# Performance work log

Measured on AMD Instinct MI355X. Metric: run time of the kernel, lower is better.

The kernel has to match this reference:

```python
import jax, jax.numpy as jnp
import numpy as np

B, S, D_IN, D_OUT, H = 16, 1024, 768, 768, 12
HD = D_OUT // H


def setup_inputs() -> dict:
    key = jax.random.key(0)
    ks = jax.random.split(key, 6)
    s_in = D_IN ** -0.5
    s_out = D_OUT ** -0.5
    return {
        "x": jax.random.normal(ks[0], (B, S, D_IN), dtype=jnp.float32),
        "w_q": jax.random.normal(ks[1], (D_IN, D_OUT), dtype=jnp.float32) * s_in,
        "w_k": jax.random.normal(ks[2], (D_IN, D_OUT), dtype=jnp.float32) * s_in,
        "w_v": jax.random.normal(ks[3], (D_IN, D_OUT), dtype=jnp.float32) * s_in,
        "w_o": jax.random.normal(ks[4], (D_OUT, D_OUT), dtype=jnp.float32) * s_out,
        "b_o": jax.random.normal(ks[5], (D_OUT,), dtype=jnp.float32) * 0.01,
    }


def reference(x, w_q, w_k, w_v, w_o, b_o):
    b, s, _ = x.shape
    # QKV projections (no bias), reshape to (b, h, s, hd)
    q = (x @ w_q).reshape(b, s, H, HD).transpose(0, 2, 1, 3)
    k = (x @ w_k).reshape(b, s, H, HD).transpose(0, 2, 1, 3)
    v = (x @ w_v).reshape(b, s, H, HD).transpose(0, 2, 1, 3)
    scale = HD ** -0.5
    scores = jnp.einsum("bhqd,bhkd->bhqk", q, k) * scale
    weights = jax.nn.softmax(scores, axis=-1)  # dropout p=0.0 -> identity
    ctx = jnp.einsum("bhqk,bhkd->bhqd", weights, v)
    ctx = ctx.transpose(0, 2, 1, 3).reshape(b, s, D_OUT)
    return ctx @ w_o + b_o
```

## Files before the change

### kernel.cpp

```cpp
#include <hip/hip_runtime.h>
#include <math.h>

#define BB 16
#define SS 1024
#define DIN 768
#define DOUT 768
#define NH 12
#define HDIM 64

typedef float  f32x4  __attribute__((ext_vector_type(4)));
typedef short  bf16x8 __attribute__((ext_vector_type(8)));
typedef unsigned short u16x4 __attribute__((ext_vector_type(4)));

__device__ __forceinline__ unsigned short f2b(float f) {
    union { float f; unsigned u; } v; v.f = f;
    unsigned r = v.u + 0x7FFFu + ((v.u >> 16) & 1u);
    return (unsigned short)(r >> 16);
}

__global__ __launch_bounds__(256) void k_convert_x(
    const float* __restrict__ x, unsigned short* __restrict__ xb, int n4)
{
    for (int i = blockIdx.x * 256 + threadIdx.x; i < n4; i += gridDim.x * 256) {
        float4 v = reinterpret_cast<const float4*>(x)[i];
        u16x4 o;
        o[0] = f2b(v.x); o[1] = f2b(v.y); o[2] = f2b(v.z); o[3] = f2b(v.w);
        reinterpret_cast<u16x4*>(xb)[i] = o;
    }
}

__global__ __launch_bounds__(256) void k_convert_w(
    const float* __restrict__ wq, const float* __restrict__ wk,
    const float* __restrict__ wv, const float* __restrict__ wo,
    unsigned short* __restrict__ wt, unsigned short* __restrict__ wot)
{
    __shared__ float T[64][65];
    const int z = blockIdx.z;
    const float* in = (z == 0) ? wq : (z == 1) ? wk : (z == 2) ? wv : wo;
    unsigned short* out = (z < 3) ? (wt + z * DIN * DOUT) : wot;

    const int k0 = blockIdx.x * 64;
    const int n0 = blockIdx.y * 64;
    const int tid = threadIdx.x;

    for (int i = tid; i < 4096; i += 256) {
        int r = i >> 6, c = i & 63;
        T[r][c] = in[(k0 + r) * DOUT + n0 + c];
    }
    __syncthreads();
    for (int i = tid; i < 4096; i += 256) {
        int r = i >> 6, c = i & 63;
        out[(n0 + r) * DIN + k0 + c] = f2b(T[c][r]);
    }
}

__global__ __launch_bounds__(256) void k_qkv_gemm(
    const unsigned short* __restrict__ A,
    const unsigned short* __restrict__ wt,
    unsigned short* __restrict__ qo, unsigned short* __restrict__ ko,
    unsigned short* __restrict__ vo)
{
    __shared__ unsigned short As[128 * 64];
    __shared__ unsigned short Bs[128 * 64];

    const int z = blockIdx.z;
    const unsigned short* Bt = wt + z * DIN * DOUT;
    unsigned short* outb = (z == 0) ? qo : (z == 1) ? ko : vo;

    const int tid  = threadIdx.x;
    const int lane = tid & 63;
    const int wid  = tid >> 6;
    const int wm   = wid >> 1, wn = wid & 1;
    const int lr   = lane & 15, lg = lane >> 4;

    const int m0 = blockIdx.x * 128;
    const int n0 = blockIdx.y * 128;

    f32x4 acc[4][4];
    #pragma unroll
    for (int i = 0; i < 4; ++i)
        #pragma unroll
        for (int j = 0; j < 4; ++j) acc[i][j] = (f32x4){0.f, 0.f, 0.f, 0.f};

    for (int kt = 0; kt < DIN / 64; ++kt) {
        const int k0 = kt * 64;
        #pragma unroll
        for (int t = 0; t < 4; ++t) {
            int c = tid + t * 256;
            int r = c >> 3, ch = c & 7;
            *reinterpret_cast<bf16x8*>(&As[(r << 6) + ((ch ^ (r & 7)) << 3)]) =
                *reinterpret_cast<const bf16x8*>(&A[(m0 + r) * DIN + k0 + (ch << 3)]);
            *reinterpret_cast<bf16x8*>(&Bs[(r << 6) + ((ch ^ (r & 7)) << 3)]) =
                *reinterpret_cast<const bf16x8*>(&Bt[(n0 + r) * DIN + k0 + (ch << 3)]);
        }
        __syncthreads();

        #pragma unroll
        for (int ks = 0; ks < 2; ++ks) {
            bf16x8 af[4], bfr[4];
            #pragma unroll
            for (int mi = 0; mi < 4; ++mi) {
                int r = wm * 64 + mi * 16 + lr;
                af[mi] = *reinterpret_cast<const bf16x8*>(
                    &As[(r << 6) + ((((ks << 2) + lg) ^ (r & 7)) << 3)]);
            }
            #pragma unroll
            for (int ni = 0; ni < 4; ++ni) {
                int r = wn * 64 + ni * 16 + lr;
                bfr[ni] = *reinterpret_cast<const bf16x8*>(
                    &Bs[(r << 6) + ((((ks << 2) + lg) ^ (r & 7)) << 3)]);
            }
            #pragma unroll
            for (int mi = 0; mi < 4; ++mi)
                #pragma unroll
                for (int ni = 0; ni < 4; ++ni)
                    acc[mi][ni] = __builtin_amdgcn_mfma_f32_16x16x32_bf16(
                        af[mi], bfr[ni], acc[mi][ni], 0, 0, 0);
        }
        __syncthreads();
    }

    #pragma unroll
    for (int mi = 0; mi < 4; ++mi) {
        #pragma unroll
        for (int rg = 0; rg < 4; ++rg) {
            int m = m0 + wm * 64 + mi * 16 + lg * 4 + rg;
            int b = m >> 10, s = m & 1023;
            #pragma unroll
            for (int ni = 0; ni < 4; ++ni) {
                int n = n0 + wn * 64 + ni * 16 + lr;
                int h = n >> 6, hd = n & 63;
                outb[((b * NH + h) * SS + s) * HDIM + hd] = f2b(acc[mi][ni][rg]);
            }
        }
    }
}

__global__ __launch_bounds__(256) void k_vtrans(
    const unsigned short* __restrict__ vb, unsigned short* __restrict__ vt)
{
    __shared__ unsigned short T[64 * 72];
    const int tid = threadIdx.x;
    const int st  = blockIdx.x;
    const int bh  = blockIdx.y;
    const int base = bh << 16;

    #pragma unroll
    for (int t = 0; t < 2; ++t) {
        int c = tid + t * 256;
        int s = c >> 3, d0 = (c & 7) << 3;
        *reinterpret_cast<bf16x8*>(&T[s * 72 + d0]) =
            *reinterpret_cast<const bf16x8*>(&vb[base + ((st * 64 + s) << 6) + d0]);
    }
    __syncthreads();
    #pragma unroll
    for (int t = 0; t < 2; ++t) {
        int c = tid + t * 256;
        int d = c >> 3, s0 = (c & 7) << 3;
        bf16x8 o;
        #pragma unroll
        for (int i = 0; i < 8; ++i) o[i] = (short)T[(s0 + i) * 72 + d];
        *reinterpret_cast<bf16x8*>(&vt[base + (d << 10) + st * 64 + s0]) = o;
    }
}

__global__ __launch_bounds__(256) void k_attn(
    const unsigned short* __restrict__ qb, const unsigned short* __restrict__ kb,
    const unsigned short* __restrict__ vt, unsigned short* __restrict__ ctxb)
{
    __shared__ unsigned short Qs[64 * 64];
    __shared__ unsigned short Ks[64 * 64];
    __shared__ unsigned short Vs[64 * 64];
    __shared__ unsigned short Ps[64 * 64];

    const int tid  = threadIdx.x;
    const int lane = tid & 63;
    const int w    = tid >> 6;
    const int lr   = lane & 15, lg = lane >> 4;
    const int qt   = blockIdx.x;
    const int bh   = blockIdx.y;
    const int b    = bh / NH, h = bh % NH;
    const int base = bh << 16;

    #pragma unroll
    for (int t = 0; t < 2; ++t) {
        int c = tid + t * 256;
        int r = c >> 3, ch = c & 7;
        *reinterpret_cast<bf16x8*>(&Qs[(r << 6) + ((ch ^ (r & 7)) << 3)]) =
            *reinterpret_cast<const bf16x8*>(&qb[base + ((qt * 64 + r) << 6) + (ch << 3)]);
    }

    float m_r[4], l_r[4];
    f32x4 ctx[4];
    #pragma unroll
    for (int i = 0; i < 4; ++i) {
        m_r[i] = -INFINITY; l_r[i] = 0.f;
        ctx[i] = (f32x4){0.f, 0.f, 0.f, 0.f};
    }

    for (int kt = 0; kt < 16; ++kt) {
        #pragma unroll
        for (int t = 0; t < 2; ++t) {
            int c = tid + t * 256;
            int r = c >> 3, ch = c & 7;
            *reinterpret_cast<bf16x8*>(&Ks[(r << 6) + ((ch ^ (r & 7)) << 3)]) =
                *reinterpret_cast<const bf16x8*>(&kb[base + ((kt * 64 + r) << 6) + (ch << 3)]);
            *reinterpret_cast<bf16x8*>(&Vs[(r << 6) + ((ch ^ (r & 7)) << 3)]) =
                *reinterpret_cast<const bf16x8*>(&vt[base + (r << 10) + (kt << 6) + (ch << 3)]);
        }
        __syncthreads();

        f32x4 sc[4];
        #pragma unroll
        for (int ni = 0; ni < 4; ++ni) sc[ni] = (f32x4){0.f, 0.f, 0.f, 0.f};
        #pragma unroll
        for (int ks = 0; ks < 2; ++ks) {
            int qrow = (w << 4) + lr;
            bf16x8 aq = *reinterpret_cast<const bf16x8*>(
                &Qs[(qrow << 6) + ((((ks << 2) + lg) ^ (qrow & 7)) << 3)]);
            #pragma unroll
            for (int ni = 0; ni < 4; ++ni) {
                int krow = (ni << 4) + lr;
                bf16x8 bk = *reinterpret_cast<const bf16x8*>(
                    &Ks[(krow << 6) + ((((ks << 2) + lg) ^ (krow & 7)) << 3)]);
                sc[ni] = __builtin_amdgcn_mfma_f32_16x16x32_bf16(aq, bk, sc[ni], 0, 0, 0);
            }
        }
        #pragma unroll
        for (int ni = 0; ni < 4; ++ni) sc[ni] *= 0.125f;

        #pragma unroll
        for (int rg = 0; rg < 4; ++rg) {
            float mx = fmaxf(fmaxf(sc[0][rg], sc[1][rg]),
                             fmaxf(sc[2][rg], sc[3][rg]));
            #pragma unroll
            for (int o = 1; o < 16; o <<= 1) mx = fmaxf(mx, __shfl_xor(mx, o));
            float mnew = fmaxf(m_r[rg], mx);
            float corr = __expf(m_r[rg] - mnew);
            float rs = 0.f;
            #pragma unroll
            for (int ni = 0; ni < 4; ++ni) {
                float p = __expf(sc[ni][rg] - mnew);
                sc[ni][rg] = p; rs += p;
            }
            #pragma unroll
            for (int o = 1; o < 16; o <<= 1) rs += __shfl_xor(rs, o);
            l_r[rg] = l_r[rg] * corr + rs;
            m_r[rg] = mnew;
            #pragma unroll
            for (int di = 0; di < 4; ++di) ctx[di][rg] *= corr;
        }

        #pragma unroll
        for (int rg = 0; rg < 4; ++rg) {
            int qr = (w << 4) + (lg << 2) + rg;
            #pragma unroll
            for (int ni = 0; ni < 4; ++ni) {
                int key = (ni << 4) + lr;
                Ps[(qr << 6) + ((((key >> 3) ^ (qr & 7)) << 3)) + (key & 7)]
                    = f2b(sc[ni][rg]);
            }
        }

        #pragma unroll
        for (int ks = 0; ks < 2; ++ks) {
            int prow = (w << 4) + lr;
            bf16x8 ap = *reinterpret_cast<const bf16x8*>(
                &Ps[(prow << 6) + ((((ks << 2) + lg) ^ (prow & 7)) << 3)]);
            #pragma unroll
            for (int di = 0; di < 4; ++di) {
                int vrow = (di << 4) + lr;
                bf16x8 bv = *reinterpret_cast<const bf16x8*>(
                    &Vs[(vrow << 6) + ((((ks << 2) + lg) ^ (vrow & 7)) << 3)]);
                ctx[di] = __builtin_amdgcn_mfma_f32_16x16x32_bf16(ap, bv, ctx[di], 0, 0, 0);
            }
        }
        __syncthreads();
    }

    #pragma unroll
    for (int rg = 0; rg < 4; ++rg) {
        float inv = 1.f / l_r[rg];
        int q = (qt << 6) + (w << 4) + (lg << 2) + rg;
        #pragma unroll
        for (int di = 0; di < 4; ++di) {
            int d = (di << 4) + lr;
            ctxb[(b * SS + q) * DOUT + h * HDIM + d] = f2b(ctx[di][rg] * inv);
        }
    }
}

__global__ __launch_bounds__(256) void k_out_gemm(
    const unsigned short* __restrict__ A,
    const unsigned short* __restrict__ Bt,
    const float* __restrict__ bo, float* __restrict__ out)
{
    __shared__ unsigned short As[128 * 64];
    __shared__ unsigned short Bs[128 * 64];

    const int tid  = threadIdx.x;
    const int lane = tid & 63;
    const int wid  = tid >> 6;
    const int wm   = wid >> 1, wn = wid & 1;
    const int lr   = lane & 15, lg = lane >> 4;

    const int m0 = blockIdx.x * 128;
    const int n0 = blockIdx.y * 128;

    f32x4 acc[4][4];
    #pragma unroll
    for (int i = 0; i < 4; ++i)
        #pragma unroll
        for (int j = 0; j < 4; ++j) acc[i][j] = (f32x4){0.f, 0.f, 0.f, 0.f};

    for (int kt = 0; kt < DOUT / 64; ++kt) {
        const int k0 = kt * 64;
        #pragma unroll
        for (int t = 0; t < 4; ++t) {
            int c = tid + t * 256;
            int r = c >> 3, ch = c & 7;
            *reinterpret_cast<bf16x8*>(&As[(r << 6) + ((ch ^ (r & 7)) << 3)]) =
                *reinterpret_cast<const bf16x8*>(&A[(m0 + r) * DOUT + k0 + (ch << 3)]);
            *reinterpret_cast<bf16x8*>(&Bs[(r << 6) + ((ch ^ (r & 7)) << 3)]) =
                *reinterpret_cast<const bf16x8*>(&Bt[(n0 + r) * DOUT + k0 + (ch << 3)]);
        }
        __syncthreads();

        #pragma unroll
        for (int ks = 0; ks < 2; ++ks) {
            bf16x8 af[4], bfr[4];
            #pragma unroll
            for (int mi = 0; mi < 4; ++mi) {
                int r = wm * 64 + mi * 16 + lr;
                af[mi] = *reinterpret_cast<const bf16x8*>(
                    &As[(r << 6) + ((((ks << 2) + lg) ^ (r & 7)) << 3)]);
            }
            #pragma unroll
            for (int ni = 0; ni < 4; ++ni) {
                int r = wn * 64 + ni * 16 + lr;
                bfr[ni] = *reinterpret_cast<const bf16x8*>(
                    &Bs[(r << 6) + ((((ks << 2) + lg) ^ (r & 7)) << 3)]);
            }
            #pragma unroll
            for (int mi = 0; mi < 4; ++mi)
                #pragma unroll
                for (int ni = 0; ni < 4; ++ni)
                    acc[mi][ni] = __builtin_amdgcn_mfma_f32_16x16x32_bf16(
                        af[mi], bfr[ni], acc[mi][ni], 0, 0, 0);
        }
        __syncthreads();
    }

    #pragma unroll
    for (int mi = 0; mi < 4; ++mi) {
        #pragma unroll
        for (int rg = 0; rg < 4; ++rg) {
            int m = m0 + wm * 64 + mi * 16 + lg * 4 + rg;
            #pragma unroll
            for (int ni = 0; ni < 4; ++ni) {
                int n = n0 + wn * 64 + ni * 16 + lr;
                out[m * DOUT + n] = acc[mi][ni][rg] + bo[n];
            }
        }
    }
}

extern "C" void kernel_launch(void* const* d_in, const int* in_sizes, int n_in,
                              void* d_out, int out_size, void* d_ws, size_t ws_size,
                              hipStream_t stream)
{
    const float* x  = (const float*)d_in[0];
    const float* wq = (const float*)d_in[1];
    const float* wk = (const float*)d_in[2];
    const float* wv = (const float*)d_in[3];
    const float* wo = (const float*)d_in[4];
    const float* bo = (const float*)d_in[5];
    float* out = (float*)d_out;

    const size_t N_X   = (size_t)BB * SS * DIN;
    const size_t N_W   = (size_t)DIN * DOUT;
    const size_t N_BHSD= (size_t)BB * NH * SS * HDIM;

    unsigned short* xb   = (unsigned short*)d_ws;
    unsigned short* wt   = xb   + N_X;
    unsigned short* wot  = wt   + 3 * N_W;
    unsigned short* qbuf = wot  + N_W;
    unsigned short* kbuf = qbuf + N_BHSD;
    unsigned short* vbuf = kbuf + N_BHSD;
    unsigned short* vtb  = vbuf + N_BHSD;
    unsigned short* ctxb = vtb  + N_BHSD;

    size_t need = (N_X + 4 * N_W + 5 * N_BHSD) * sizeof(unsigned short);
    if (ws_size < need) return;

    k_convert_x<<<4096, 256, 0, stream>>>(x, xb, (int)(N_X / 4));
    k_convert_w<<<dim3(12, 12, 4), 256, 0, stream>>>(wq, wk, wv, wo, wt, wot);
    k_qkv_gemm<<<dim3(128, 6, 3), 256, 0, stream>>>(xb, wt, qbuf, kbuf, vbuf);
    k_vtrans<<<dim3(16, 192), 256, 0, stream>>>(vbuf, vtb);
    k_attn<<<dim3(16, 192), 256, 0, stream>>>(qbuf, kbuf, vtb, ctxb);
    k_out_gemm<<<dim3(128, 6), 256, 0, stream>>>(ctxb, wot, bo, out);
}
```

Baseline: 401.0 us.

## Rework attention with 32x32 MFMA, direct-to-LDS loads, and fused V transpose

```diff
diff --git a/kernel.cpp b/kernel.cpp
--- a/kernel.cpp
+++ b/kernel.cpp
@@ -8,8 +8,9 @@
 #define NH 12
 #define HDIM 64
 
-typedef float  f32x4  __attribute__((ext_vector_type(4)));
-typedef short  bf16x8 __attribute__((ext_vector_type(8)));
+typedef float  f32x4   __attribute__((ext_vector_type(4)));
+typedef float  f32x16  __attribute__((ext_vector_type(16)));
+typedef short  bf16x8  __attribute__((ext_vector_type(8)));
 typedef unsigned short u16x4 __attribute__((ext_vector_type(4)));
 
 __device__ __forceinline__ unsigned short f2b(float f) {
@@ -17,6 +18,10 @@
     unsigned r = v.u + 0x7FFFu + ((v.u >> 16) & 1u);
     return (unsigned short)(r >> 16);
 }
+
+#define GLOAD16(gp, lp) __builtin_amdgcn_global_load_lds( \
+    (const __attribute__((address_space(1))) void*)(gp),  \
+    (__attribute__((address_space(3))) void*)(lp), 16, 0, 0)
 
 __global__ __launch_bounds__(256) void k_convert_x(
     const float* __restrict__ x, unsigned short* __restrict__ xb, int n4)
@@ -37,7 +42,7 @@
     __shared__ float T[64][65];
     const int z = blockIdx.z;
     const float* in = (z == 0) ? wq : (z == 1) ? wk : (z == 2) ? wv : wo;
-    unsigned short* out = (z < 3) ? (wt + z * DIN * DOUT) : wot;
+    unsigned short* out = (z < 3) ? (wt + (size_t)z * DIN * DOUT) : wot;
 
     const int k0 = blockIdx.x * 64;
     const int n0 = blockIdx.y * 64;
@@ -50,7 +55,7 @@
     __syncthreads();
     for (int i = tid; i < 4096; i += 256) {
         int r = i >> 6, c = i & 63;
-        out[(n0 + r) * DIN + k0 + c] = f2b(T[c][r]);
+        out[(size_t)(n0 + r) * DIN + k0 + c] = f2b(T[c][r]);
     }
 }
 
@@ -58,14 +63,13 @@
     const unsigned short* __restrict__ A,
     const unsigned short* __restrict__ wt,
     unsigned short* __restrict__ qo, unsigned short* __restrict__ ko,
-    unsigned short* __restrict__ vo)
+    unsigned short* __restrict__ vtb)
 {
     __shared__ unsigned short As[128 * 64];
     __shared__ unsigned short Bs[128 * 64];
 
     const int z = blockIdx.z;
-    const unsigned short* Bt = wt + z * DIN * DOUT;
-    unsigned short* outb = (z == 0) ? qo : (z == 1) ? ko : vo;
+    const unsigned short* Bt = wt + (size_t)z * DIN * DOUT;
 
     const int tid  = threadIdx.x;
     const int lane = tid & 63;
@@ -86,12 +90,13 @@
         const int k0 = kt * 64;
         #pragma unroll
         for (int t = 0; t < 4; ++t) {
-            int c = tid + t * 256;
-            int r = c >> 3, ch = c & 7;
-            *reinterpret_cast<bf16x8*>(&As[(r << 6) + ((ch ^ (r & 7)) << 3)]) =
-                *reinterpret_cast<const bf16x8*>(&A[(m0 + r) * DIN + k0 + (ch << 3)]);
-            *reinterpret_cast<bf16x8*>(&Bs[(r << 6) + ((ch ^ (r & 7)) << 3)]) =
-                *reinterpret_cast<const bf16x8*>(&Bt[(n0 + r) * DIN + k0 + (ch << 3)]);
+            int c  = t * 256 + wid * 64 + lane;
+            int r  = c >> 3;
+            int ch = (c & 7) ^ (r & 7);
+            GLOAD16(&A[(size_t)(m0 + r) * DIN + k0 + (ch << 3)],
+                    &As[(t * 256 + wid * 64) * 8]);
+            GLOAD16(&Bt[(size_t)(n0 + r) * DIN + k0 + (ch << 3)],
+                    &Bs[(t * 256 + wid * 64) * 8]);
         }
         __syncthreads();
 
@@ -120,6 +125,7 @@
         __syncthreads();
     }
 
+    const float oscale = (z == 0) ? 0.125f : 1.0f;
     #pragma unroll
     for (int mi = 0; mi < 4; ++mi) {
         #pragma unroll
@@ -130,37 +136,15 @@
             for (int ni = 0; ni < 4; ++ni) {
                 int n = n0 + wn * 64 + ni * 16 + lr;
                 int h = n >> 6, hd = n & 63;
-                outb[((b * NH + h) * SS + s) * HDIM + hd] = f2b(acc[mi][ni][rg]);
-            }
-        }
-    }
-}
-
-__global__ __launch_bounds__(256) void k_vtrans(
-    const unsigned short* __restrict__ vb, unsigned short* __restrict__ vt)
-{
-    __shared__ unsigned short T[64 * 72];
-    const int tid = threadIdx.x;
-    const int st  = blockIdx.x;
-    const int bh  = blockIdx.y;
-    const int base = bh << 16;
-
-    #pragma unroll
-    for (int t = 0; t < 2; ++t) {
-        int c = tid + t * 256;
-        int s = c >> 3, d0 = (c & 7) << 3;
-        *reinterpret_cast<bf16x8*>(&T[s * 72 + d0]) =
-            *reinterpret_cast<const bf16x8*>(&vb[base + ((st * 64 + s) << 6) + d0]);
-    }
-    __syncthreads();
-    #pragma unroll
-    for (int t = 0; t < 2; ++t) {
-        int c = tid + t * 256;
-        int d = c >> 3, s0 = (c & 7) << 3;
-        bf16x8 o;
-        #pragma unroll
-        for (int i = 0; i < 8; ++i) o[i] = (short)T[(s0 + i) * 72 + d];
-        *reinterpret_cast<bf16x8*>(&vt[base + (d << 10) + st * 64 + s0]) = o;
+                unsigned short val = f2b(acc[mi][ni][rg] * oscale);
+                if (z == 2) {
+                    vtb[(((size_t)(b * NH + h)) << 16) + (hd << 10) + s] = val;
+                } else {
+                    unsigned short* ob = (z == 0) ? qo : ko;
+                    ob[(((size_t)(b * NH + h) * SS + s) << 6) + hd] = val;
+                }
+            }
+        }
     }
 }
 
@@ -168,125 +152,130 @@
     const unsigned short* __restrict__ qb, const unsigned short* __restrict__ kb,
     const unsigned short* __restrict__ vt, unsigned short* __restrict__ ctxb)
 {
-    __shared__ unsigned short Qs[64 * 64];
     __shared__ unsigned short Ks[64 * 64];
     __shared__ unsigned short Vs[64 * 64];
-    __shared__ unsigned short Ps[64 * 64];
 
     const int tid  = threadIdx.x;
     const int lane = tid & 63;
     const int w    = tid >> 6;
-    const int lr   = lane & 15, lg = lane >> 4;
+    const int h    = lane >> 5;
+    const int q31  = lane & 31;
     const int qt   = blockIdx.x;
     const int bh   = blockIdx.y;
-    const int b    = bh / NH, h = bh % NH;
-    const int base = bh << 16;
-
-    #pragma unroll
-    for (int t = 0; t < 2; ++t) {
-        int c = tid + t * 256;
-        int r = c >> 3, ch = c & 7;
-        *reinterpret_cast<bf16x8*>(&Qs[(r << 6) + ((ch ^ (r & 7)) << 3)]) =
-            *reinterpret_cast<const bf16x8*>(&qb[base + ((qt * 64 + r) << 6) + (ch << 3)]);
-    }
-
-    float m_r[4], l_r[4];
-    f32x4 ctx[4];
-    #pragma unroll
-    for (int i = 0; i < 4; ++i) {
-        m_r[i] = -INFINITY; l_r[i] = 0.f;
-        ctx[i] = (f32x4){0.f, 0.f, 0.f, 0.f};
-    }
+    const int bb   = bh / NH, hh = bh % NH;
+    const size_t base = (size_t)bh << 16;
+
+    const int q_glob = qt * 128 + w * 32 + q31;
+
+    bf16x8 qf[4];
+    #pragma unroll
+    for (int kk = 0; kk < 4; ++kk)
+        qf[kk] = *reinterpret_cast<const bf16x8*>(
+            &qb[base + ((size_t)q_glob << 6) + (kk << 4) + (h << 3)]);
+
+    float m_run = -INFINITY, l_run = 0.f;
+    f32x16 ctx0, ctx1;
+    #pragma unroll
+    for (int i = 0; i < 16; ++i) { ctx0[i] = 0.f; ctx1[i] = 0.f; }
 
     for (int kt = 0; kt < 16; ++kt) {
         #pragma unroll
         for (int t = 0; t < 2; ++t) {
-            int c = tid + t * 256;
-            int r = c >> 3, ch = c & 7;
-            *reinterpret_cast<bf16x8*>(&Ks[(r << 6) + ((ch ^ (r & 7)) << 3)]) =
-                *reinterpret_cast<const bf16x8*>(&kb[base + ((kt * 64 + r) << 6) + (ch << 3)]);
-            *reinterpret_cast<bf16x8*>(&Vs[(r << 6) + ((ch ^ (r & 7)) << 3)]) =
-                *reinterpret_cast<const bf16x8*>(&vt[base + (r << 10) + (kt << 6) + (ch << 3)]);
-        }
-        __syncthreads();
-
-        f32x4 sc[4];
-        #pragma unroll
-        for (int ni = 0; ni < 4; ++ni) sc[ni] = (f32x4){0.f, 0.f, 0.f, 0.f};
-        #pragma unroll
-        for (int ks = 0; ks < 2; ++ks) {
-            int qrow = (w << 4) + lr;
-            bf16x8 aq = *reinterpret_cast<const bf16x8*>(
-                &Qs[(qrow << 6) + ((((ks << 2) + lg) ^ (qrow & 7)) << 3)]);
-            #pragma unroll
-            for (int ni = 0; ni < 4; ++ni) {
-                int krow = (ni << 4) + lr;
-                bf16x8 bk = *reinterpret_cast<const bf16x8*>(
-                    &Ks[(krow << 6) + ((((ks << 2) + lg) ^ (krow & 7)) << 3)]);
-                sc[ni] = __builtin_amdgcn_mfma_f32_16x16x32_bf16(aq, bk, sc[ni], 0, 0, 0);
-            }
-        }
-        #pragma unroll
-        for (int ni = 0; ni < 4; ++ni) sc[ni] *= 0.125f;
-
-        #pragma unroll
-        for (int rg = 0; rg < 4; ++rg) {
-            float mx = fmaxf(fmaxf(sc[0][rg], sc[1][rg]),
-                             fmaxf(sc[2][rg], sc[3][rg]));
-            #pragma unroll
-            for (int o = 1; o < 16; o <<= 1) mx = fmaxf(mx, __shfl_xor(mx, o));
-            float mnew = fmaxf(m_r[rg], mx);
-            float corr = __expf(m_r[rg] - mnew);
-            float rs = 0.f;
-            #pragma unroll
-            for (int ni = 0; ni < 4; ++ni) {
-                float p = __expf(sc[ni][rg] - mnew);
-                sc[ni][rg] = p; rs += p;
-            }
-            #pragma unroll
-            for (int o = 1; o < 16; o <<= 1) rs += __shfl_xor(rs, o);
-            l_r[rg] = l_r[rg] * corr + rs;
-            m_r[rg] = mnew;
-            #pragma unroll
-            for (int di = 0; di < 4; ++di) ctx[di][rg] *= corr;
-        }
-
-        #pragma unroll
-        for (int rg = 0; rg < 4; ++rg) {
-            int qr = (w << 4) + (lg << 2) + rg;
-            #pragma unroll
-            for (int ni = 0; ni < 4; ++ni) {
-                int key = (ni << 4) + lr;
-                Ps[(qr << 6) + ((((key >> 3) ^ (qr & 7)) << 3)) + (key & 7)]
-                    = f2b(sc[ni][rg]);
-            }
-        }
-
-        #pragma unroll
-        for (int ks = 0; ks < 2; ++ks) {
-            int prow = (w << 4) + lr;
-            bf16x8 ap = *reinterpret_cast<const bf16x8*>(
-                &Ps[(prow << 6) + ((((ks << 2) + lg) ^ (prow & 7)) << 3)]);
-            #pragma unroll
-            for (int di = 0; di < 4; ++di) {
-                int vrow = (di << 4) + lr;
-                bf16x8 bv = *reinterpret_cast<const bf16x8*>(
-                    &Vs[(vrow << 6) + ((((ks << 2) + lg) ^ (vrow & 7)) << 3)]);
-                ctx[di] = __builtin_amdgcn_mfma_f32_16x16x32_bf16(ap, bv, ctx[di], 0, 0, 0);
-            }
-        }
-        __syncthreads();
-    }
-
-    #pragma unroll
-    for (int rg = 0; rg < 4; ++rg) {
-        float inv = 1.f / l_r[rg];
-        int q = (qt << 6) + (w << 4) + (lg << 2) + rg;
-        #pragma unroll
-        for (int di = 0; di < 4; ++di) {
-            int d = (di << 4) + lr;
-            ctxb[(b * SS + q) * DOUT + h * HDIM + d] = f2b(ctx[di][rg] * inv);
-        }
+            int c  = t * 256 + w * 64 + lane;
+            int r  = c >> 3;
+            int ch = (c & 7) ^ (r & 7);
+            GLOAD16(&kb[base + ((size_t)(kt * 64 + r) << 6) + (ch << 3)],
+                    &Ks[(t * 256 + w * 64) * 8]);
+            GLOAD16(&vt[base + ((size_t)r << 10) + (kt << 6) + (ch << 3)],
+                    &Vs[(t * 256 + w * 64) * 8]);
+        }
+        __syncthreads();
+
+        f32x16 sc0, sc1;
+        #pragma unroll
+        for (int i = 0; i < 16; ++i) { sc0[i] = 0.f; sc1[i] = 0.f; }
+        #pragma unroll
+        for (int kk = 0; kk < 4; ++kk) {
+            int ch = (kk << 1) + h;
+            int r0 = q31, r1 = q31 + 32;
+            bf16x8 kf0 = *reinterpret_cast<const bf16x8*>(
+                &Ks[(r0 << 6) + ((ch ^ (r0 & 7)) << 3)]);
+            bf16x8 kf1 = *reinterpret_cast<const bf16x8*>(
+                &Ks[(r1 << 6) + ((ch ^ (r1 & 7)) << 3)]);
+            sc0 = __builtin_amdgcn_mfma_f32_32x32x16_bf16(kf0, qf[kk], sc0, 0, 0, 0);
+            sc1 = __builtin_amdgcn_mfma_f32_32x32x16_bf16(kf1, qf[kk], sc1, 0, 0, 0);
+        }
+
+        float mx = fmaxf(sc0[0], sc1[0]);
+        #pragma unroll
+        for (int i = 1; i < 16; ++i) mx = fmaxf(mx, fmaxf(sc0[i], sc1[i]));
+        mx = fmaxf(mx, __shfl_xor(mx, 32));
+        float mnew = fmaxf(m_run, mx);
+        float corr = __expf(m_run - mnew);
+        float p0[16], p1[16];
+        float rs = 0.f;
+        #pragma unroll
+        for (int i = 0; i < 16; ++i) {
+            p0[i] = __expf(sc0[i] - mnew); rs += p0[i];
+            p1[i] = __expf(sc1[i] - mnew); rs += p1[i];
+        }
+        rs += __shfl_xor(rs, 32);
+        l_run = l_run * corr + rs;
+        m_run = mnew;
+        #pragma unroll
+        for (int i = 0; i < 16; ++i) { ctx0[i] *= corr; ctx1[i] *= corr; }
+
+        unsigned pk0[8], pk1[8];
+        #pragma unroll
+        for (int j = 0; j < 8; ++j) {
+            pk0[j] = (unsigned)f2b(p0[2 * j]) | ((unsigned)f2b(p0[2 * j + 1]) << 16);
+            pk1[j] = (unsigned)f2b(p1[2 * j]) | ((unsigned)f2b(p1[2 * j + 1]) << 16);
+        }
+
+        #pragma unroll
+        for (int kk = 0; kk < 4; ++kk) {
+            unsigned a0, a1, b0, b1;
+            if (kk < 2) {
+                a0 = pk0[4 * (kk & 1)];     a1 = pk0[4 * (kk & 1) + 1];
+                b0 = pk0[4 * (kk & 1) + 2]; b1 = pk0[4 * (kk & 1) + 3];
+            } else {
+                a0 = pk1[4 * (kk & 1)];     a1 = pk1[4 * (kk & 1) + 1];
+                b0 = pk1[4 * (kk & 1) + 2]; b1 = pk1[4 * (kk & 1) + 3];
+            }
+            unsigned mine0 = h ? b0 : a0, mine1 = h ? b1 : a1;
+            unsigned give0 = h ? a0 : b0, give1 = h ? a1 : b1;
+            unsigned sw0 = (unsigned)__shfl_xor((int)give0, 32);
+            unsigned sw1 = (unsigned)__shfl_xor((int)give1, 32);
+            union { unsigned u[4]; bf16x8 v; } pf;
+            pf.u[0] = h ? sw0 : mine0;
+            pf.u[1] = h ? sw1 : mine1;
+            pf.u[2] = h ? mine0 : sw0;
+            pf.u[3] = h ? mine1 : sw1;
+
+            int ch = (kk << 1) + h;
+            int d0 = q31, d1 = q31 + 32;
+            bf16x8 vf0 = *reinterpret_cast<const bf16x8*>(
+                &Vs[(d0 << 6) + ((ch ^ (d0 & 7)) << 3)]);
+            bf16x8 vf1 = *reinterpret_cast<const bf16x8*>(
+                &Vs[(d1 << 6) + ((ch ^ (d1 & 7)) << 3)]);
+            ctx0 = __builtin_amdgcn_mfma_f32_32x32x16_bf16(vf0, pf.v, ctx0, 0, 0, 0);
+            ctx1 = __builtin_amdgcn_mfma_f32_32x32x16_bf16(vf1, pf.v, ctx1, 0, 0, 0);
+        }
+        __syncthreads();
+    }
+
+    float inv = 1.f / l_run;
+    size_t obase = ((size_t)(bb * SS + q_glob)) * DOUT + hh * HDIM;
+    #pragma unroll
+    for (int g = 0; g < 4; ++g) {
+        u16x4 o0, o1;
+        #pragma unroll
+        for (int e = 0; e < 4; ++e) {
+            o0[e] = f2b(ctx0[4 * g + e] * inv);
+            o1[e] = f2b(ctx1[4 * g + e] * inv);
+        }
+        *reinterpret_cast<u16x4*>(&ctxb[obase + 8 * g + 4 * h])      = o0;
+        *reinterpret_cast<u16x4*>(&ctxb[obase + 8 * g + 4 * h + 32]) = o1;
     }
 }
 
@@ -317,12 +306,13 @@
         const int k0 = kt * 64;
         #pragma unroll
         for (int t = 0; t < 4; ++t) {
-            int c = tid + t * 256;
-            int r = c >> 3, ch = c & 7;
-            *reinterpret_cast<bf16x8*>(&As[(r << 6) + ((ch ^ (r & 7)) << 3)]) =
-                *reinterpret_cast<const bf16x8*>(&A[(m0 + r) * DOUT + k0 + (ch << 3)]);
-            *reinterpret_cast<bf16x8*>(&Bs[(r << 6) + ((ch ^ (r & 7)) << 3)]) =
-                *reinterpret_cast<const bf16x8*>(&Bt[(n0 + r) * DOUT + k0 + (ch << 3)]);
+            int c  = t * 256 + wid * 64 + lane;
+            int r  = c >> 3;
+            int ch = (c & 7) ^ (r & 7);
+            GLOAD16(&A[(size_t)(m0 + r) * DOUT + k0 + (ch << 3)],
+                    &As[(t * 256 + wid * 64) * 8]);
+            GLOAD16(&Bt[(size_t)(n0 + r) * DOUT + k0 + (ch << 3)],
+                    &Bs[(t * 256 + wid * 64) * 8]);
         }
         __syncthreads();
 
@@ -359,7 +349,7 @@
             #pragma unroll
             for (int ni = 0; ni < 4; ++ni) {
                 int n = n0 + wn * 64 + ni * 16 + lr;
-                out[m * DOUT + n] = acc[mi][ni][rg] + bo[n];
+                out[(size_t)m * DOUT + n] = acc[mi][ni][rg] + bo[n];
             }
         }
     }
@@ -377,26 +367,24 @@
     const float* bo = (const float*)d_in[5];
     float* out = (float*)d_out;
 
-    const size_t N_X   = (size_t)BB * SS * DIN;
-    const size_t N_W   = (size_t)DIN * DOUT;
-    const size_t N_BHSD= (size_t)BB * NH * SS * HDIM;
+    const size_t N_X    = (size_t)BB * SS * DIN;
+    const size_t N_W    = (size_t)DIN * DOUT;
+    const size_t N_BHSD = (size_t)BB * NH * SS * HDIM;
 
     unsigned short* xb   = (unsigned short*)d_ws;
     unsigned short* wt   = xb   + N_X;
     unsigned short* wot  = wt   + 3 * N_W;
     unsigned short* qbuf = wot  + N_W;
     unsigned short* kbuf = qbuf + N_BHSD;
-    unsigned short* vbuf = kbuf + N_BHSD;
-    unsigned short* vtb  = vbuf + N_BHSD;
+    unsigned short* vtb  = kbuf + N_BHSD;
     unsigned short* ctxb = vtb  + N_BHSD;
 
-    size_t need = (N_X + 4 * N_W + 5 * N_BHSD) * sizeof(unsigned short);
+    size_t need = (N_X + 4 * N_W + 4 * N_BHSD) * sizeof(unsigned short);
     if (ws_size < need) return;
 
     k_convert_x<<<4096, 256, 0, stream>>>(x, xb, (int)(N_X / 4));
     k_convert_w<<<dim3(12, 12, 4), 256, 0, stream>>>(wq, wk, wv, wo, wt, wot);
-    k_qkv_gemm<<<dim3(128, 6, 3), 256, 0, stream>>>(xb, wt, qbuf, kbuf, vbuf);
-    k_vtrans<<<dim3(16, 192), 256, 0, stream>>>(vbuf, vtb);
-    k_attn<<<dim3(16, 192), 256, 0, stream>>>(qbuf, kbuf, vtb, ctxb);
+    k_qkv_gemm<<<dim3(128, 6, 3), 256, 0, stream>>>(xb, wt, qbuf, kbuf, vtb);
+    k_attn<<<dim3(8, 192), 256, 0, stream>>>(qbuf, kbuf, vtb, ctxb);
     k_out_gemm<<<dim3(128, 6), 256, 0, stream>>>(ctxb, wot, bo, out);
 }
```

Result: faster. 355.0 us (-11.5%).
